# Kernel optimization log

Hardware: AMD Instinct MI355X
Metric: run time of the kernel (lower is better)

The kernel has to match this reference:

```python
import jax, jax.numpy as jnp
import numpy as np

EMB = 1024
HEAD = 64

def setup_inputs() -> dict:
    key = jax.random.key(0)
    ks = jax.random.split(key, 7)
    s = 1.0 / np.sqrt(EMB)
    x = jax.random.normal(ks[0], (4, 2048, EMB), dtype=jnp.float32)
    Wq = jax.random.uniform(ks[1], (EMB, HEAD), jnp.float32, -s, s)
    bq = jax.random.uniform(ks[2], (HEAD,), jnp.float32, -s, s)
    Wk = jax.random.uniform(ks[3], (EMB, HEAD), jnp.float32, -s, s)
    bk = jax.random.uniform(ks[4], (HEAD,), jnp.float32, -s, s)
    Wv = jax.random.uniform(ks[5], (EMB, HEAD), jnp.float32, -s, s)
    bv = jax.random.uniform(ks[6], (HEAD,), jnp.float32, -s, s)
    return {"x": x, "Wq": Wq, "bq": bq, "Wk": Wk, "bk": bk, "Wv": Wv, "bv": bv}

def reference(x, Wq, bq, Wk, bk, Wv, bv):
    x = x.astype(jnp.float32)
    q = jnp.einsum('bse,ed->bsd', x, Wq) + bq  # [B,S,H]
    k = jnp.einsum('bse,ed->bsd', x, Wk) + bk
    v = jnp.einsum('bse,ed->bsd', x, Wv) + bv
    scale = 1.0 / jnp.sqrt(jnp.asarray(k.shape[-1], jnp.float32))
    scores = jnp.einsum('bqd,bkd->bqk', q, k) * scale  # [B,S,S]
    attn = jax.nn.softmax(scores, axis=-1)
    return jnp.einsum('bqk,bkd->bqd', attn, v)  # [B,S,H]
```

## Files before the change

kernel.cpp:

```cpp
#include <hip/hip_runtime.h>
#include <hip/hip_bf16.h>

#define ROWS_TOTAL 8192
#define EMB 1024
#define HEAD 64
#define SEQ 2048
#define NWAVE 8
#define KCHUNK (SEQ / NWAVE)

typedef __attribute__((ext_vector_type(8))) short short8;
typedef __attribute__((ext_vector_type(4))) float f32x4;

#define MFMA16(a, b, c) __builtin_amdgcn_mfma_f32_16x16x32_bf16((a), (b), (c), 0, 0, 0)

static __device__ __forceinline__ unsigned short f2bf(float f) {
    union { float f; unsigned u; } v; v.f = f;
    unsigned r = v.u + 0x7fff + ((v.u >> 16) & 1);
    return (unsigned short)(r >> 16);
}

static __device__ __forceinline__ unsigned pk2(float a, float b) {
    __hip_bfloat162 h = __float22bfloat162_rn(float2{a, b});
    union { __hip_bfloat162 h; unsigned u; } v; v.h = h;
    return v.u;
}

__global__ __launch_bounds__(256) void wprep_kernel(
    const float* __restrict__ Wq, const float* __restrict__ Wk,
    const float* __restrict__ Wv, unsigned short* __restrict__ Wt)
{
    __shared__ float Tr[64][65];
    const int m  = blockIdx.y;
    const int k0 = blockIdx.x * 64;
    const float* __restrict__ W = (m == 0) ? Wq : (m == 1) ? Wk : Wv;
    const int t = threadIdx.x;

    #pragma unroll
    for (int j = 0; j < 4; ++j) {
        int flat = j * 1024 + t * 4;
        int k = flat >> 6, n = flat & 63;
        float4 w4 = *(const float4*)&W[(size_t)(k0 + k) * 64 + n];
        Tr[n + 0][k] = w4.x; Tr[n + 1][k] = w4.y;
        Tr[n + 2][k] = w4.z; Tr[n + 3][k] = w4.w;
    }
    __syncthreads();

    const int n  = t >> 2;
    const int kc = (t & 3) * 16;
    union { short8 s; unsigned u[4]; } o0, o1;
    #pragma unroll
    for (int i = 0; i < 4; ++i) {
        o0.u[i] = pk2(Tr[n][kc + 2 * i],     Tr[n][kc + 2 * i + 1]);
        o1.u[i] = pk2(Tr[n][kc + 8 + 2 * i], Tr[n][kc + 9 + 2 * i]);
    }
    unsigned short* dst = &Wt[((size_t)m * 64 + n) * 1024 + k0 + kc];
    *(short8*)(dst)     = o0.s;
    *(short8*)(dst + 8) = o1.s;
}

__global__ __launch_bounds__(512) void qkv_mfma(
    const float* __restrict__ x, const unsigned short* __restrict__ Wt,
    const float* __restrict__ bq, const float* __restrict__ bk,
    const float* __restrict__ bv,
    unsigned short* __restrict__ Qb, unsigned short* __restrict__ Kb,
    unsigned short* __restrict__ Vt)
{
    __shared__ f32x4 pr[4][3][64];
    __shared__ unsigned short vlds[64][20];

    const int t    = threadIdx.x;
    const int w    = t >> 6;
    const int lane = t & 63;
    const int ln   = lane & 15;
    const int quad = lane >> 4;
    const int m0   = blockIdx.x * 16;
    const int cg   = w >> 1;
    const int kh   = w & 1;

    const f32x4 zero = (f32x4){0.f, 0.f, 0.f, 0.f};
    f32x4 acc[3];
    #pragma unroll
    for (int j = 0; j < 3; ++j) acc[j] = zero;

    const float* __restrict__ xrow = x + (size_t)(m0 + ln) * EMB + kh * 512;
    const unsigned short* __restrict__ wbase =
        Wt + (size_t)(cg * 48 + ln) * 1024 + kh * 512 + quad * 8;

    #pragma unroll 2
    for (int kc = 0; kc < 512; kc += 32) {
        float4 a0 = *(const float4*)&xrow[kc + quad * 8];
        float4 a1 = *(const float4*)&xrow[kc + quad * 8 + 4];
        union { short8 s; unsigned u[4]; } af;
        af.u[0] = pk2(a0.x, a0.y);
        af.u[1] = pk2(a0.z, a0.w);
        af.u[2] = pk2(a1.x, a1.y);
        af.u[3] = pk2(a1.z, a1.w);
        #pragma unroll
        for (int j = 0; j < 3; ++j) {
            short8 bf = *(const short8*)&wbase[(size_t)j * 16 * 1024 + kc];
            acc[j] = MFMA16(af.s, bf, acc[j]);
        }
    }

    if (kh == 1) {
        #pragma unroll
        for (int j = 0; j < 3; ++j) pr[cg][j][lane] = acc[j];
    }
    __syncthreads();

    if (kh == 0) {
        const float qs = 0.125f * 1.44269504f;
        #pragma unroll
        for (int j = 0; j < 3; ++j) {
            acc[j] += pr[cg][j][lane];
            const int tile = cg * 3 + j;
            const int mat  = tile >> 2;
            const int d    = (tile & 3) * 16 + ln;
            const float* bp = (mat == 0) ? bq : (mat == 1) ? bk : bv;
            const float bias = bp[d];
            #pragma unroll
            for (int r = 0; r < 4; ++r) {
                float vfull = acc[j][r] + bias;
                int row = m0 + quad * 4 + r;
                if (mat == 0)      Qb[(size_t)row * 64 + d] = f2bf(vfull * qs);
                else if (mat == 1) Kb[(size_t)row * 64 + d] = f2bf(vfull);
                else               vlds[d][quad * 4 + r] = f2bf(vfull);
            }
        }
    }
    __syncthreads();

    if (t < 256) {
        const int b  = m0 >> 11;
        const int s0 = m0 & 2047;
        const int d  = t >> 2;
        const int sq = (t & 3) * 4;
        ushort4 pk = {vlds[d][sq + 0], vlds[d][sq + 1],
                      vlds[d][sq + 2], vlds[d][sq + 3]};
        *(ushort4*)&Vt[((size_t)b * 64 + d) * SEQ + s0 + sq] = pk;
    }
}

__global__ __launch_bounds__(512) void attn_mfma(
    const unsigned short* __restrict__ Qb, const unsigned short* __restrict__ Kb,
    const unsigned short* __restrict__ Vt,
    float* __restrict__ out)
{
    __shared__ float          Olds[NWAVE][16][66];
    __shared__ unsigned short Plds[NWAVE][16][72];
    __shared__ float          llds[NWAVE][16];

    const int t    = threadIdx.x;
    const int w    = t >> 6;
    const int lane = t & 63;
    const int ln   = lane & 15;
    const int quad = lane >> 4;

    const int q0 = blockIdx.x * 16;
    const int b  = q0 >> 11;

    const unsigned short* qbase = Qb + (size_t)(q0 + ln) * 64 + quad * 8;
    short8 qa0 = *(const short8*)(qbase);
    short8 qa1 = *(const short8*)(qbase + 32);

    const f32x4 zero = (f32x4){0.f, 0.f, 0.f, 0.f};
    f32x4 O[4];
    #pragma unroll
    for (int j = 0; j < 4; ++j) O[j] = zero;
    float lacc[4] = {0.f, 0.f, 0.f, 0.f};

    const unsigned short* Kbase = Kb + ((size_t)b * SEQ + w * KCHUNK) * 64;
    const unsigned short* Vbase = Vt + (size_t)b * 64 * SEQ + w * KCHUNK;
    unsigned short* P = &Plds[w][0][0];

    #pragma unroll 2
    for (int kt = 0; kt < KCHUNK; kt += 64) {
        const unsigned short* kr = Kbase + (size_t)(kt + ln) * 64 + quad * 8;
        short8 kA0 = *(const short8*)(kr);
        short8 kA1 = *(const short8*)(kr + 32);
        short8 kB0 = *(const short8*)(kr + 16 * 64);
        short8 kB1 = *(const short8*)(kr + 16 * 64 + 32);
        short8 kC0 = *(const short8*)(kr + 32 * 64);
        short8 kC1 = *(const short8*)(kr + 32 * 64 + 32);
        short8 kD0 = *(const short8*)(kr + 48 * 64);
        short8 kD1 = *(const short8*)(kr + 48 * 64 + 32);

        f32x4 sA = MFMA16(qa0, kA0, zero); sA = MFMA16(qa1, kA1, sA);
        f32x4 sB = MFMA16(qa0, kB0, zero); sB = MFMA16(qa1, kB1, sB);
        f32x4 sC = MFMA16(qa0, kC0, zero); sC = MFMA16(qa1, kC1, sC);
        f32x4 sD = MFMA16(qa0, kD0, zero); sD = MFMA16(qa1, kD1, sD);

        #pragma unroll
        for (int r = 0; r < 4; ++r) {
            float pA = __builtin_amdgcn_exp2f(sA[r]);
            float pB = __builtin_amdgcn_exp2f(sB[r]);
            float pC = __builtin_amdgcn_exp2f(sC[r]);
            float pD = __builtin_amdgcn_exp2f(sD[r]);
            lacc[r] += (pA + pB) + (pC + pD);
            unsigned uAB = pk2(pA, pB);
            unsigned uCD = pk2(pC, pD);
            unsigned short* prow = P + (quad * 4 + r) * 72;
            prow[ln]      = (unsigned short)uAB;
            prow[16 + ln] = (unsigned short)(uAB >> 16);
            prow[32 + ln] = (unsigned short)uCD;
            prow[48 + ln] = (unsigned short)(uCD >> 16);
        }
        short8 pa0 = *(const short8*)&Plds[w][ln][quad * 8];
        short8 pa1 = *(const short8*)&Plds[w][ln][32 + quad * 8];

        #pragma unroll
        for (int j = 0; j < 4; ++j) {
            const unsigned short* vr =
                Vbase + (size_t)(j * 16 + ln) * SEQ + kt + quad * 8;
            short8 vb0 = *(const short8*)(vr);
            short8 vb1 = *(const short8*)(vr + 32);
            O[j] = MFMA16(pa0, vb0, O[j]);
            O[j] = MFMA16(pa1, vb1, O[j]);
        }
    }

    #pragma unroll
    for (int m = 1; m < 16; m <<= 1) {
        #pragma unroll
        for (int r = 0; r < 4; ++r) lacc[r] += __shfl_xor(lacc[r], m);
    }

    #pragma unroll
    for (int j = 0; j < 4; ++j)
        #pragma unroll
        for (int r = 0; r < 4; ++r)
            Olds[w][quad * 4 + r][j * 16 + ln] = O[j][r];
    if (ln == 0) {
        #pragma unroll
        for (int r = 0; r < 4; ++r) llds[w][quad * 4 + r] = lacc[r];
    }
    __syncthreads();

    {
        const int idx = t * 2;
        const int row = idx >> 6;
        const int d   = idx & 63;
        float lsum = 0.f, o0 = 0.f, o1 = 0.f;
        #pragma unroll
        for (int v = 0; v < NWAVE; ++v) {
            lsum += llds[v][row];
            o0   += Olds[v][row][d];
            o1   += Olds[v][row][d + 1];
        }
        float inv = 1.0f / lsum;
        float2 res = {o0 * inv, o1 * inv};
        *(float2*)&out[(size_t)(q0 + row) * 64 + d] = res;
    }
}

extern "C" void kernel_launch(void* const* d_in, const int* in_sizes, int n_in,
                              void* d_out, int out_size, void* d_ws, size_t ws_size,
                              hipStream_t stream)
{
    const float* x  = (const float*)d_in[0];
    const float* Wq = (const float*)d_in[1];
    const float* bq = (const float*)d_in[2];
    const float* Wk = (const float*)d_in[3];
    const float* bk = (const float*)d_in[4];
    const float* Wv = (const float*)d_in[5];
    const float* bv = (const float*)d_in[6];
    float* out = (float*)d_out;

    char* ws = (char*)d_ws;
    unsigned short* Qb = (unsigned short*)ws;
    unsigned short* Kb = Qb + (size_t)ROWS_TOTAL * HEAD;
    unsigned short* Vt = Kb + (size_t)ROWS_TOTAL * HEAD;
    unsigned short* Wt = Vt + (size_t)ROWS_TOTAL * HEAD;

    wprep_kernel<<<dim3(16, 3), 256, 0, stream>>>(Wq, Wk, Wv, Wt);
    qkv_mfma<<<dim3(512), 512, 0, stream>>>(x, Wt, bq, bk, bv, Qb, Kb, Vt);
    attn_mfma<<<dim3(512), 512, 0, stream>>>(Qb, Kb, Vt, out);
}
```

Baseline: 147.7 us.

## Share K/V tiles in LDS across query waves and split keys across blocks

The attention kernel now gives each block 128 queries (8 waves of 16) and one of 8 key chunks. Each 64-key K and V tile is staged cooperatively in LDS and reused by all 8 waves, where before every wave streamed its own K/V from global memory. The 8 key-chunk partials are written to a workspace, and a new reduce kernel sums them and normalises. This cuts redundant global K/V reads at the cost of two barriers per tile, an extra kernel launch, and partial-output traffic through global memory.

```diff
diff --git a/kernel.cpp b/kernel.cpp
--- a/kernel.cpp
+++ b/kernel.cpp
@@ -5,8 +5,9 @@
 #define EMB 1024
 #define HEAD 64
 #define SEQ 2048
-#define NWAVE 8
-#define KCHUNK (SEQ / NWAVE)
+#define KSPLIT 8
+#define KC (SEQ / KSPLIT)
+#define KT 64
 
 typedef __attribute__((ext_vector_type(8))) short short8;
 typedef __attribute__((ext_vector_type(4))) float f32x4;
@@ -144,11 +145,11 @@
 __global__ __launch_bounds__(512) void attn_mfma(
     const unsigned short* __restrict__ Qb, const unsigned short* __restrict__ Kb,
     const unsigned short* __restrict__ Vt,
-    float* __restrict__ out)
-{
-    __shared__ float          Olds[NWAVE][16][66];
-    __shared__ unsigned short Plds[NWAVE][16][72];
-    __shared__ float          llds[NWAVE][16];
+    float* __restrict__ Opart, float* __restrict__ lpart)
+{
+    __shared__ unsigned short Kl[KT][72];
+    __shared__ unsigned short Vl[HEAD][72];
+    __shared__ unsigned short Plds[8][16][72];
 
     const int t    = threadIdx.x;
     const int w    = t >> 6;
@@ -156,8 +157,9 @@
     const int ln   = lane & 15;
     const int quad = lane >> 4;
 
-    const int q0 = blockIdx.x * 16;
-    const int b  = q0 >> 11;
+    const int c  = blockIdx.y;
+    const int q0 = blockIdx.x * 128 + w * 16;
+    const int b  = blockIdx.x >> 4;
 
     const unsigned short* qbase = Qb + (size_t)(q0 + ln) * 64 + quad * 8;
     short8 qa0 = *(const short8*)(qbase);
@@ -169,54 +171,55 @@
     for (int j = 0; j < 4; ++j) O[j] = zero;
     float lacc[4] = {0.f, 0.f, 0.f, 0.f};
 
-    const unsigned short* Kbase = Kb + ((size_t)b * SEQ + w * KCHUNK) * 64;
-    const unsigned short* Vbase = Vt + (size_t)b * 64 * SEQ + w * KCHUNK;
+    const int skey = t >> 3;
+    const int soff = (t & 7) * 8;
+    const unsigned short* Ksrc =
+        Kb + ((size_t)b * SEQ + c * KC + skey) * 64 + soff;
+    const unsigned short* Vsrc =
+        Vt + ((size_t)b * 64 + skey) * SEQ + c * KC + soff;
+
     unsigned short* P = &Plds[w][0][0];
 
-    #pragma unroll 2
-    for (int kt = 0; kt < KCHUNK; kt += 64) {
-        const unsigned short* kr = Kbase + (size_t)(kt + ln) * 64 + quad * 8;
-        short8 kA0 = *(const short8*)(kr);
-        short8 kA1 = *(const short8*)(kr + 32);
-        short8 kB0 = *(const short8*)(kr + 16 * 64);
-        short8 kB1 = *(const short8*)(kr + 16 * 64 + 32);
-        short8 kC0 = *(const short8*)(kr + 32 * 64);
-        short8 kC1 = *(const short8*)(kr + 32 * 64 + 32);
-        short8 kD0 = *(const short8*)(kr + 48 * 64);
-        short8 kD1 = *(const short8*)(kr + 48 * 64 + 32);
-
-        f32x4 sA = MFMA16(qa0, kA0, zero); sA = MFMA16(qa1, kA1, sA);
-        f32x4 sB = MFMA16(qa0, kB0, zero); sB = MFMA16(qa1, kB1, sB);
-        f32x4 sC = MFMA16(qa0, kC0, zero); sC = MFMA16(qa1, kC1, sC);
-        f32x4 sD = MFMA16(qa0, kD0, zero); sD = MFMA16(qa1, kD1, sD);
+    for (int kt = 0; kt < KC; kt += KT) {
+        *(short8*)&Kl[skey][soff] = *(const short8*)(Ksrc + (size_t)kt * 64);
+        *(short8*)&Vl[skey][soff] = *(const short8*)(Vsrc + kt);
+        __syncthreads();
+
+        f32x4 s[4];
+        #pragma unroll
+        for (int sub = 0; sub < 4; ++sub) {
+            short8 kb0 = *(const short8*)&Kl[sub * 16 + ln][quad * 8];
+            short8 kb1 = *(const short8*)&Kl[sub * 16 + ln][32 + quad * 8];
+            s[sub] = MFMA16(qa0, kb0, zero);
+            s[sub] = MFMA16(qa1, kb1, s[sub]);
+        }
 
         #pragma unroll
         for (int r = 0; r < 4; ++r) {
-            float pA = __builtin_amdgcn_exp2f(sA[r]);
-            float pB = __builtin_amdgcn_exp2f(sB[r]);
-            float pC = __builtin_amdgcn_exp2f(sC[r]);
-            float pD = __builtin_amdgcn_exp2f(sD[r]);
-            lacc[r] += (pA + pB) + (pC + pD);
-            unsigned uAB = pk2(pA, pB);
-            unsigned uCD = pk2(pC, pD);
+            float p0 = __builtin_amdgcn_exp2f(s[0][r]);
+            float p1 = __builtin_amdgcn_exp2f(s[1][r]);
+            float p2 = __builtin_amdgcn_exp2f(s[2][r]);
+            float p3 = __builtin_amdgcn_exp2f(s[3][r]);
+            lacc[r] += (p0 + p1) + (p2 + p3);
+            unsigned u01 = pk2(p0, p1);
+            unsigned u23 = pk2(p2, p3);
             unsigned short* prow = P + (quad * 4 + r) * 72;
-            prow[ln]      = (unsigned short)uAB;
-            prow[16 + ln] = (unsigned short)(uAB >> 16);
-            prow[32 + ln] = (unsigned short)uCD;
-            prow[48 + ln] = (unsigned short)(uCD >> 16);
+            prow[ln]      = (unsigned short)u01;
+            prow[16 + ln] = (unsigned short)(u01 >> 16);
+            prow[32 + ln] = (unsigned short)u23;
+            prow[48 + ln] = (unsigned short)(u23 >> 16);
         }
         short8 pa0 = *(const short8*)&Plds[w][ln][quad * 8];
         short8 pa1 = *(const short8*)&Plds[w][ln][32 + quad * 8];
 
         #pragma unroll
         for (int j = 0; j < 4; ++j) {
-            const unsigned short* vr =
-                Vbase + (size_t)(j * 16 + ln) * SEQ + kt + quad * 8;
-            short8 vb0 = *(const short8*)(vr);
-            short8 vb1 = *(const short8*)(vr + 32);
+            short8 vb0 = *(const short8*)&Vl[j * 16 + ln][quad * 8];
+            short8 vb1 = *(const short8*)&Vl[j * 16 + ln][32 + quad * 8];
             O[j] = MFMA16(pa0, vb0, O[j]);
             O[j] = MFMA16(pa1, vb1, O[j]);
         }
+        __syncthreads();
     }
 
     #pragma unroll
@@ -225,32 +228,33 @@
         for (int r = 0; r < 4; ++r) lacc[r] += __shfl_xor(lacc[r], m);
     }
 
+    float* __restrict__ ob = Opart + ((size_t)c * ROWS_TOTAL + q0) * 64;
     #pragma unroll
     for (int j = 0; j < 4; ++j)
         #pragma unroll
         for (int r = 0; r < 4; ++r)
-            Olds[w][quad * 4 + r][j * 16 + ln] = O[j][r];
+            ob[(size_t)(quad * 4 + r) * 64 + j * 16 + ln] = O[j][r];
+
     if (ln == 0) {
         #pragma unroll
-        for (int r = 0; r < 4; ++r) llds[w][quad * 4 + r] = lacc[r];
-    }
-    __syncthreads();
-
-    {
-        const int idx = t * 2;
-        const int row = idx >> 6;
-        const int d   = idx & 63;
-        float lsum = 0.f, o0 = 0.f, o1 = 0.f;
-        #pragma unroll
-        for (int v = 0; v < NWAVE; ++v) {
-            lsum += llds[v][row];
-            o0   += Olds[v][row][d];
-            o1   += Olds[v][row][d + 1];
-        }
-        float inv = 1.0f / lsum;
-        float2 res = {o0 * inv, o1 * inv};
-        *(float2*)&out[(size_t)(q0 + row) * 64 + d] = res;
-    }
+        for (int r = 0; r < 4; ++r)
+            lpart[(size_t)c * ROWS_TOTAL + q0 + quad * 4 + r] = lacc[r];
+    }
+}
+
+__global__ __launch_bounds__(256) void reduce_kernel(
+    const float* __restrict__ Opart, const float* __restrict__ lpart,
+    float* __restrict__ out)
+{
+    const int idx = blockIdx.x * 256 + threadIdx.x;
+    const int r   = idx >> 6;
+    float osum = 0.f, lsum = 0.f;
+    #pragma unroll
+    for (int c = 0; c < KSPLIT; ++c) {
+        osum += Opart[(size_t)c * ROWS_TOTAL * HEAD + idx];
+        lsum += lpart[(size_t)c * ROWS_TOTAL + r];
+    }
+    out[idx] = osum / lsum;
 }
 
 extern "C" void kernel_launch(void* const* d_in, const int* in_sizes, int n_in,
@@ -271,8 +275,11 @@
     unsigned short* Kb = Qb + (size_t)ROWS_TOTAL * HEAD;
     unsigned short* Vt = Kb + (size_t)ROWS_TOTAL * HEAD;
     unsigned short* Wt = Vt + (size_t)ROWS_TOTAL * HEAD;
+    float* lpart = (float*)(Wt + (size_t)3 * HEAD * EMB);
+    float* Opart = lpart + (size_t)KSPLIT * ROWS_TOTAL;
 
     wprep_kernel<<<dim3(16, 3), 256, 0, stream>>>(Wq, Wk, Wv, Wt);
     qkv_mfma<<<dim3(512), 512, 0, stream>>>(x, Wt, bq, bk, bv, Qb, Kb, Vt);
-    attn_mfma<<<dim3(512), 512, 0, stream>>>(Qb, Kb, Vt, out);
-}
+    attn_mfma<<<dim3(64, KSPLIT), 512, 0, stream>>>(Qb, Kb, Vt, Opart, lpart);
+    reduce_kernel<<<dim3((ROWS_TOTAL * HEAD) / 256), 256, 0, stream>>>(Opart, lpart, out);
+}
```

Result: faster. 134.9 us (-8.7%).
